# Kernel optimization log

Hardware: AMD Instinct MI355X
Metric: run time of the kernel (lower is better)

## Reference

```python
import jax, jax.numpy as jnp
import numpy as np

D = 768          # embedding_dim
H = 12           # num_heads
DH = 768         # head_dim == embedding_dim (hardcoded in Block)
DF = 4 * D       # FFN hidden
B, S = 4, 1024
EPS = 1e-5


def setup_inputs() -> dict:
    key = jax.random.key(0)
    ks = jax.random.split(key, 20)
    sd = lambda fan_in: 1.0 / np.sqrt(fan_in)
    return {
        "x":  jax.random.normal(ks[0], (B, S, D), jnp.float32),
        # per-head QKV (stacked over head axis)
        "Wq": jax.random.normal(ks[1], (H, D, DH), jnp.float32) * sd(D),
        "bq": jnp.zeros((H, DH), jnp.float32),
        "Wk": jax.random.normal(ks[2], (H, D, DH), jnp.float32) * sd(D),
        "bk": jnp.zeros((H, DH), jnp.float32),
        "Wv": jax.random.normal(ks[3], (H, D, DH), jnp.float32) * sd(D),
        "bv": jnp.zeros((H, DH), jnp.float32),
        # output projection: concat(H*DH) -> D
        "Wo": jax.random.normal(ks[4], (H * DH, D), jnp.float32) * sd(H * DH),
        "bo": jnp.zeros((D,), jnp.float32),
        # feed-forward
        "W1": jax.random.normal(ks[5], (D, DF), jnp.float32) * sd(D),
        "b1": jnp.zeros((DF,), jnp.float32),
        "W2": jax.random.normal(ks[6], (DF, D), jnp.float32) * sd(DF),
        "b2": jnp.zeros((D,), jnp.float32),
        # layer norms
        "g1": jnp.ones((D,), jnp.float32),  "be1": jnp.zeros((D,), jnp.float32),
        "g2": jnp.ones((D,), jnp.float32),  "be2": jnp.zeros((D,), jnp.float32),
    }


def _layernorm(x, g, b):
    mu = jnp.mean(x, axis=-1, keepdims=True)
    var = jnp.mean(jnp.square(x - mu), axis=-1, keepdims=True)
    return (x - mu) * jax.lax.rsqrt(var + EPS) * g + b


def reference(x, Wq, bq, Wk, bk, Wv, bv, Wo, bo, W1, b1, W2, b2, g1, be1, g2, be2):
    h = _layernorm(x, g1, be1)                                   # [B,S,D]
    # per-head projections, stacked over head axis -> [B,H,S,DH]
    Q = jnp.einsum('bsd,hde->bhse', h, Wq) + bq[None, :, None, :]
    K = jnp.einsum('bsd,hde->bhse', h, Wk) + bk[None, :, None, :]
    V = jnp.einsum('bsd,hde->bhse', h, Wv) + bv[None, :, None, :]
    scale = DH ** -0.5
    scores = jnp.einsum('bhse,bhte->bhst', Q, K) * scale          # [B,H,S,S] (no causal mask in source)
    attn = jax.nn.softmax(scores, axis=-1)
    ctx = jnp.einsum('bhst,bhte->bhse', attn, V)                  # [B,H,S,DH]
    concat = ctx.transpose(0, 2, 1, 3).reshape(B, S, H * DH)      # concat heads on last dim
    attn_out = concat @ Wo + bo                                   # dropout: eval identity
    x1 = x + attn_out
    h2 = _layernorm(x1, g2, be2)
    ffn = jax.nn.relu(h2 @ W1 + b1) @ W2 + b2                     # dropout: eval identity
    return x1 + ffn
```

## Files before the change

kernel.cpp:

```cpp
#include <hip/hip_runtime.h>
#include <hip/hip_bf16.h>


typedef __attribute__((ext_vector_type(8))) __bf16 bf16x8;
typedef __attribute__((ext_vector_type(4))) float f32x4;
typedef __attribute__((ext_vector_type(4))) float float4_t;
typedef __attribute__((ext_vector_type(4))) unsigned short ushort4_t;

#define DEV __device__ __forceinline__

DEV unsigned short f2bf(float f) {
    __hip_bfloat16 h = __float2bfloat16(f);
    return *reinterpret_cast<unsigned short*>(&h);
}
DEV float bf2f(unsigned short u) {
    return __uint_as_float(((unsigned int)u) << 16);
}

DEV void gld16(const void* g, void* l) {
    __builtin_amdgcn_global_load_lds(
        (const __attribute__((address_space(1))) void*)g,
        (__attribute__((address_space(3))) void*)l, 16, 0, 0);
}

__global__ __launch_bounds__(256) void f2b_conv(
    const float* __restrict__ in, unsigned short* __restrict__ outb, int n4)
{
    int i = blockIdx.x * 256 + threadIdx.x;
    if (i >= n4) return;
    float4_t v = *(const float4_t*)(in + (size_t)i * 4);
    ushort4_t o;
#pragma unroll
    for (int j = 0; j < 4; j++) o[j] = f2bf(v[j]);
    *(ushort4_t*)(outb + (size_t)i * 4) = o;
}

__global__ __launch_bounds__(256) void transpose_f2b(
    const float* __restrict__ in, unsigned short* __restrict__ outb, int R, int C)
{
    __shared__ float tile[32][33];
    const int c0 = blockIdx.x * 32, r0 = blockIdx.y * 32;
    const int tx = threadIdx.x & 31, ty = threadIdx.x >> 5;
#pragma unroll
    for (int i = 0; i < 32; i += 8)
        tile[ty + i][tx] = in[(size_t)(r0 + ty + i) * C + c0 + tx];
    __syncthreads();
#pragma unroll
    for (int i = 0; i < 32; i += 8)
        outb[(size_t)(c0 + ty + i) * R + r0 + tx] = f2bf(tile[tx][ty + i]);
}

__global__ __launch_bounds__(256) void wk_bq(
    const float* __restrict__ Wk, const float* __restrict__ bq, float* __restrict__ U)
{
    int i = blockIdx.x * 256 + threadIdx.x;
    int h = i / 768;
    const float* wr = Wk + (size_t)i * 768;
    const float* bh = bq + (size_t)h * 768;
    float s = 0.f;
#pragma unroll 4
    for (int e = 0; e < 768; e++) s += wr[e] * bh[e];
    U[i] = s;
}

__global__ __launch_bounds__(256) void bvwo_part(
    const float* __restrict__ Wo, const float* __restrict__ bv, float* __restrict__ part)
{
    int e = blockIdx.x * 256 + threadIdx.x;
    int r0 = blockIdx.y * 96;
    float s = 0.f;
#pragma unroll 4
    for (int r = r0; r < r0 + 96; r++) s += bv[r] * Wo[(size_t)r * 768 + e];
    part[(size_t)blockIdx.y * 768 + e] = s;
}

__global__ __launch_bounds__(256) void bvwo_final(
    const float* __restrict__ part, const float* __restrict__ bo, float* __restrict__ R)
{
    int e = blockIdx.x * 256 + threadIdx.x;
    float s = bo[e];
#pragma unroll
    for (int c = 0; c < 96; c++) s += part[(size_t)c * 768 + e];
    R[e] = s;
}

__global__ __launch_bounds__(256) void layernorm768(
    const float* __restrict__ in, const float* __restrict__ g,
    const float* __restrict__ be, unsigned short* __restrict__ outb)
{
    const size_t rowoff = (size_t)blockIdx.x * 768;
    const float* xr = in + rowoff;
    const int t = threadIdx.x;
    float v0 = xr[t], v1 = xr[t + 256], v2 = xr[t + 512];
    __shared__ float red[8];
    float s = v0 + v1 + v2;
#pragma unroll
    for (int o = 32; o; o >>= 1) s += __shfl_down(s, o);
    if ((t & 63) == 0) red[t >> 6] = s;
    __syncthreads();
    float mu = (red[0] + red[1] + red[2] + red[3]) * (1.0f / 768.0f);
    float d0 = v0 - mu, d1 = v1 - mu, d2 = v2 - mu;
    float q = d0 * d0 + d1 * d1 + d2 * d2;
#pragma unroll
    for (int o = 32; o; o >>= 1) q += __shfl_down(q, o);
    if ((t & 63) == 0) red[4 + (t >> 6)] = q;
    __syncthreads();
    float rs = rsqrtf((red[4] + red[5] + red[6] + red[7]) * (1.0f / 768.0f) + 1e-5f);
    outb[rowoff + t]       = f2bf(d0 * rs * g[t]       + be[t]);
    outb[rowoff + t + 256] = f2bf(d1 * rs * g[t + 256] + be[t + 256]);
    outb[rowoff + t + 512] = f2bf(d2 * rs * g[t + 512] + be[t + 512]);
}

__global__ __launch_bounds__(256) void softmax1024(unsigned short* __restrict__ p)
{
    unsigned short* row = p + (size_t)blockIdx.x * 1024;
    const int t = threadIdx.x;
    ushort4_t uv = *(const ushort4_t*)(row + t * 4);
    float v[4];
    float m = -3.4e38f;
#pragma unroll
    for (int i = 0; i < 4; i++) { v[i] = bf2f(uv[i]); m = fmaxf(m, v[i]); }
    __shared__ float red[8];
#pragma unroll
    for (int o = 32; o; o >>= 1) m = fmaxf(m, __shfl_down(m, o));
    if ((t & 63) == 0) red[t >> 6] = m;
    __syncthreads();
    m = fmaxf(fmaxf(red[0], red[1]), fmaxf(red[2], red[3]));
    float s = 0.f;
#pragma unroll
    for (int i = 0; i < 4; i++) { v[i] = __expf(v[i] - m); s += v[i]; }
#pragma unroll
    for (int o = 32; o; o >>= 1) s += __shfl_down(s, o);
    if ((t & 63) == 0) red[4 + (t >> 6)] = s;
    __syncthreads();
    float inv = 1.f / (red[4] + red[5] + red[6] + red[7]);
    ushort4_t ov;
#pragma unroll
    for (int i = 0; i < 4; i++) ov[i] = f2bf(v[i] * inv);
    *(ushort4_t*)(row + t * 4) = ov;
}

__global__ __launch_bounds__(256) void reduce4(
    const float* __restrict__ res, const float* __restrict__ colb,
    const float* __restrict__ p0, const float* __restrict__ p1,
    const float* __restrict__ p2, const float* __restrict__ p3,
    float* __restrict__ dst)
{
    int i = blockIdx.x * 256 + threadIdx.x;
    float4_t r = *(const float4_t*)(res + (size_t)i * 4);
    float4_t a = *(const float4_t*)(p0 + (size_t)i * 4);
    float4_t b = *(const float4_t*)(p1 + (size_t)i * 4);
    float4_t c = *(const float4_t*)(p2 + (size_t)i * 4);
    float4_t d = *(const float4_t*)(p3 + (size_t)i * 4);
    float4_t cb = *(const float4_t*)(colb + (size_t)(i % 192) * 4);
    float4_t o;
#pragma unroll
    for (int j = 0; j < 4; j++) o[j] = r[j] + cb[j] + (a[j] + b[j]) + (c[j] + d[j]);
    *(float4_t*)(dst + (size_t)i * 4) = o;
}

enum { MODE_BF16 = 0, MODE_VT = 1, MODE_F32RES = 2 };

template <int MODE, bool RELU>
__global__ __launch_bounds__(256) void gemm_bt(
    const unsigned short* __restrict__ A, int lda,
    const unsigned short* __restrict__ Bt, int ldb,
    void* __restrict__ Cout, int ldc,
    const float* __restrict__ bias,
    const float* __restrict__ res, int ldr,
    float scale, int K, int zdiv,
    long long sA1, long long sA2, long long sB1, long long sB2,
    long long sC1, long long sC2, long long sCJ, long long sBias)
{
    const unsigned gx = gridDim.x, gy = gridDim.y;
    const unsigned nwg = gx * gy * gridDim.z;
    unsigned lin = blockIdx.x + gx * (blockIdx.y + gy * blockIdx.z);
    {
        const unsigned q = nwg >> 3, r = nwg & 7;
        const unsigned xcd = lin & 7, idx = lin >> 3;
        lin = (xcd < r ? xcd * (q + 1) : r * (q + 1) + (xcd - r) * q) + idx;
    }
    const unsigned bx = lin % gx;
    const unsigned rem = lin / gx;
    const unsigned by = rem % gy, bz = rem / gy;

    const int z = (int)bz, zq = z / zdiv, zr = z % zdiv;
    A  += (size_t)zq * sA1 + (size_t)zr * sA2;
    Bt += (size_t)zq * sB1 + (size_t)zr * sB2;
    const size_t cOff = (size_t)zq * sC1 + (size_t)(zq >> 1) * sCJ + (size_t)zr * sC2;
    const float* biasp = bias ? bias + (size_t)zr * sBias : nullptr;

    const int m0 = by * 128, n0 = bx * 128;

    __shared__ __align__(16) unsigned short As[2][128 * 32];
    __shared__ __align__(16) unsigned short Bs[2][128 * 32];

    const int t = threadIdx.x, lane = t & 63, wave = t >> 6;
    const int wr = wave >> 1, wc = wave & 1;

    f32x4 zero = {0.f, 0.f, 0.f, 0.f};
    f32x4 acc[4][4];
#pragma unroll
    for (int i = 0; i < 4; i++)
#pragma unroll
        for (int j = 0; j < 4; j++) acc[i][j] = zero;

    const int r0 = t >> 2;
    const int ce = (t & 3) * 8;
    const int kq = (lane >> 4) * 8, rr = lane & 15;

    const int nt = K >> 5;

    auto stage = [&](int buf, int kt) {
        const int kk = kt * 32;
        const unsigned short* ga0 = A  + (size_t)(m0 + r0) * lda      + kk + ce;
        const unsigned short* ga1 = A  + (size_t)(m0 + 64 + r0) * lda + kk + ce;
        const unsigned short* gb0 = Bt + (size_t)(n0 + r0) * ldb      + kk + ce;
        const unsigned short* gb1 = Bt + (size_t)(n0 + 64 + r0) * ldb + kk + ce;
        char* la = (char*)(&As[buf][0]);
        char* lb = (char*)(&Bs[buf][0]);
        gld16(ga0, la + wave * 1024);
        gld16(ga1, la + 4096 + wave * 1024);
        gld16(gb0, lb + wave * 1024);
        gld16(gb1, lb + 4096 + wave * 1024);
    };

    stage(0, 0);
    stage(1, 1);
    asm volatile("s_waitcnt vmcnt(4)" ::: "memory");
    __builtin_amdgcn_s_barrier();

    int cur = 0;
    for (int kt = 0; kt < nt; ++kt) {
        bf16x8 a[4], b[4];
        const unsigned short* Ab = &As[cur][0];
        const unsigned short* Bb = &Bs[cur][0];
#pragma unroll
        for (int i = 0; i < 4; i++) {
            a[i] = *(const bf16x8*)(Ab + (wr * 64 + i * 16 + rr) * 32 + kq);
            b[i] = *(const bf16x8*)(Bb + (wc * 64 + i * 16 + rr) * 32 + kq);
        }
        asm volatile("s_waitcnt lgkmcnt(0)" ::: "memory");
        __builtin_amdgcn_s_barrier();
        if (kt + 2 < nt) stage(cur, kt + 2);

        __builtin_amdgcn_s_setprio(1);
#pragma unroll
        for (int i = 0; i < 4; i++)
#pragma unroll
            for (int j = 0; j < 4; j++)
                acc[i][j] = __builtin_amdgcn_mfma_f32_16x16x32_bf16(a[i], b[j], acc[i][j], 0, 0, 0);
        __builtin_amdgcn_s_setprio(0);

        if (kt + 2 < nt) asm volatile("s_waitcnt vmcnt(4)" ::: "memory");
        else             asm volatile("s_waitcnt vmcnt(0)" ::: "memory");
        __builtin_amdgcn_s_barrier();
        cur ^= 1;
    }

    const int cr = (lane >> 4) * 4, cc = lane & 15;
#pragma unroll
    for (int i = 0; i < 4; i++) {
        const int rowb = m0 + wr * 64 + i * 16 + cr;
#pragma unroll
        for (int j = 0; j < 4; j++) {
            const int col = n0 + wc * 64 + j * 16 + cc;
            const float bv = biasp ? biasp[col] : 0.f;
            if (MODE == MODE_VT) {
                ushort4_t pk;
#pragma unroll
                for (int r = 0; r < 4; r++) {
                    float v = acc[i][j][r] * scale + bv;
                    if (RELU) v = fmaxf(v, 0.f);
                    pk[r] = f2bf(v);
                }
                *(ushort4_t*)((unsigned short*)Cout + cOff +
                              (size_t)col * ldc + rowb) = pk;
            } else {
#pragma unroll
                for (int r = 0; r < 4; r++) {
                    float v = acc[i][j][r] * scale + bv;
                    if (RELU) v = fmaxf(v, 0.f);
                    const int row = rowb + r;
                    if (MODE == MODE_BF16) {
                        ((unsigned short*)Cout)[cOff + (size_t)row * ldc + col] = f2bf(v);
                    } else {
                        float ov = res ? v + res[(size_t)row * ldr + col] : v;
                        ((float*)Cout)[cOff + (size_t)row * ldc + col] = ov;
                    }
                }
            }
        }
    }
}

__global__ void ws_too_small(float* o, float v) { o[0] = v; }

extern "C" void kernel_launch(void* const* d_in, const int* in_sizes, int n_in,
                              void* d_out, int out_size, void* d_ws, size_t ws_size,
                              hipStream_t stream)
{
    const float* x   = (const float*)d_in[0];
    const float* Wq  = (const float*)d_in[1];
    const float* bq  = (const float*)d_in[2];
    const float* Wk  = (const float*)d_in[3];
    const float* Wv  = (const float*)d_in[5];
    const float* bv  = (const float*)d_in[6];
    const float* Wo  = (const float*)d_in[7];
    const float* bo  = (const float*)d_in[8];
    const float* W1  = (const float*)d_in[9];
    const float* b1  = (const float*)d_in[10];
    const float* W2  = (const float*)d_in[11];
    const float* b2  = (const float*)d_in[12];
    const float* g1  = (const float*)d_in[13];
    const float* be1 = (const float*)d_in[14];
    const float* g2  = (const float*)d_in[15];
    const float* be2 = (const float*)d_in[16];
    float* out = (float*)d_out;

    char* ws = (char*)d_ws;
    unsigned short* W1T  = (unsigned short*)(ws);
    unsigned short* W2T  = (unsigned short*)(ws + 4718592);
    unsigned short* WQKT = (unsigned short*)(ws + 9437184);
    unsigned short* WVOT = (unsigned short*)(ws + 23592960);
    float*          U    = (float*)(ws + 37748736);
    float*          BVWO = (float*)(ws + 37785600);
    float*          PART = (float*)(ws + 37788672);
    unsigned short* HB   = (unsigned short*)(ws + 38083584);
    float*          X1   = (float*)(ws + 44375040);
    unsigned short* TB   = (unsigned short*)(ws + 56957952);
    unsigned short* SC   = (unsigned short*)(ws + 132455424);
    const size_t NEED = 258284544;

    if (ws_size < NEED) {
        hipMemsetAsync(d_out, 0, (size_t)out_size * sizeof(float), stream);
        ws_too_small<<<1, 1, 0, stream>>>(out, (float)ws_size);
        return;
    }

    unsigned short* VOT = TB;
    float* P0 = (float*)(ws + 9437184);
    float* P1 = (float*)(ws + 22020096);
    float* P2 = (float*)(ws + 233118720);
    float* P3 = (float*)(ws + 245701632);
    unsigned short* WqB = (unsigned short*)(ws + 132455424);
    unsigned short* WkB = (unsigned short*)(ws + 146611200);
    unsigned short* WvB = (unsigned short*)(ws + 160766976);
    unsigned short* WOT = (unsigned short*)(ws + 174922752);
    unsigned short* H2B = (unsigned short*)(ws + 56957952);
    unsigned short* FFN = (unsigned short*)(ws + 63249408);

    f2b_conv<<<6912, 256, 0, stream>>>(Wq, WqB, 1769472);
    f2b_conv<<<6912, 256, 0, stream>>>(Wk, WkB, 1769472);
    f2b_conv<<<6912, 256, 0, stream>>>(Wv, WvB, 1769472);
    transpose_f2b<<<dim3(24, 288), 256, 0, stream>>>(Wo, WOT, 9216, 768);
    transpose_f2b<<<dim3(96, 24), 256, 0, stream>>>(W1, W1T, 768, 3072);
    transpose_f2b<<<dim3(24, 96), 256, 0, stream>>>(W2, W2T, 3072, 768);

    gemm_bt<MODE_BF16, false><<<dim3(6, 6, 12), 256, 0, stream>>>(
        WkB, 768, WqB, 768, WQKT, 768, nullptr, nullptr, 0, 1.0f, 768, 12,
        0, 589824, 0, 589824, 0, 589824, 0, 0);
    gemm_bt<MODE_BF16, false><<<dim3(6, 6, 12), 256, 0, stream>>>(
        WOT, 9216, WvB, 768, WVOT, 768, nullptr, nullptr, 0, 1.0f, 768, 12,
        0, 768, 0, 589824, 0, 589824, 0, 0);

    wk_bq<<<36, 256, 0, stream>>>(Wk, bq, U);
    bvwo_part<<<dim3(3, 96), 256, 0, stream>>>(Wo, bv, PART);
    bvwo_final<<<3, 256, 0, stream>>>(PART, bo, BVWO);

    layernorm768<<<4096, 256, 0, stream>>>(x, g1, be1, HB);

    gemm_bt<MODE_BF16, false><<<dim3(6, 8, 48), 256, 0, stream>>>(
        HB, 768, WQKT, 768, TB, 768, U, nullptr, 0, 1.0f, 768, 12,
        786432, 0, 0, 589824, 9437184, 786432, 0, 768);

    gemm_bt<MODE_BF16, false><<<dim3(8, 8, 48), 256, 0, stream>>>(
        TB, 768, HB, 768, SC, 12288, nullptr, nullptr, 0,
        0.03608439182435161f, 768, 12,
        9437184, 786432, 786432, 0, 12582912, 1024, 0, 0);

    softmax1024<<<49152, 256, 0, stream>>>(SC);

    gemm_bt<MODE_VT, false><<<dim3(6, 8, 48), 256, 0, stream>>>(
        HB, 768, WVOT, 768, VOT, 12288, nullptr, nullptr, 0, 1.0f, 768, 12,
        786432, 0, 0, 589824, 9437184, 1024, 0, 0);

    gemm_bt<MODE_F32RES, false><<<dim3(6, 8, 16), 256, 0, stream>>>(
        SC, 12288, VOT, 12288, P0, 768, nullptr, nullptr, 0, 1.0f, 3072, 4,
        3072, 12582912, 3072, 9437184, 3145728, 786432, 49628928, 0);

    reduce4<<<3072, 256, 0, stream>>>(x, BVWO, P0, P1, P2, P3, X1);

    layernorm768<<<4096, 256, 0, stream>>>(X1, g2, be2, H2B);

    gemm_bt<MODE_BF16, true><<<dim3(24, 32, 1), 256, 0, stream>>>(
        H2B, 768, W1T, 768, FFN, 3072, b1, nullptr, 0, 1.0f, 768, 1,
        0, 0, 0, 0, 0, 0, 0, 0);

    gemm_bt<MODE_F32RES, false><<<dim3(6, 32, 4), 256, 0, stream>>>(
        FFN, 3072, W2T, 3072, P0, 768, nullptr, nullptr, 0, 1.0f, 768, 1,
        768, 0, 768, 0, 3145728, 0, 49628928, 0);

    reduce4<<<3072, 256, 0, stream>>>(X1, b2, P0, P1, P2, P3, out);
}
```

Measured before the change: 673.6 us.

## Add 256x256-tile 8-wave GEMM kernel with 4-stage pipeline for activation GEMMs

Adds a new bf16 MFMA GEMM kernel that uses 256x256 output tiles, 512 threads (8 waves), and a four-buffer global-to-LDS pipeline. Loads for A and B are interleaved with two MFMA half-steps, and setprio raises wave priority during the MFMA sections. All per-forward activation GEMMs switch to this kernel with correspondingly smaller grids. The larger tiles are meant to increase operand reuse and cut global traffic per FLOP, at the cost of fewer workgroups, more LDS and register pressure, and possible wave-quantization imbalance on the smaller grids.

```diff
diff --git a/kernel.cpp b/kernel.cpp
--- a/kernel.cpp
+++ b/kernel.cpp
@@ -160,6 +160,152 @@
 }
 
 enum { MODE_BF16 = 0, MODE_VT = 1, MODE_F32RES = 2 };
+
+template <int MODE, bool RELU>
+__global__ __launch_bounds__(512, 2) void gemm256(
+    const unsigned short* __restrict__ A, int lda,
+    const unsigned short* __restrict__ Bt, int ldb,
+    void* __restrict__ Cout, int ldc,
+    const float* __restrict__ bias,
+    const float* __restrict__ res, int ldr,
+    float scale, int K, int zdiv,
+    long long sA1, long long sA2, long long sB1, long long sB2,
+    long long sC1, long long sC2, long long sCJ, long long sBias)
+{
+    const unsigned gx = gridDim.x, gy = gridDim.y;
+    const unsigned nwg = gx * gy * gridDim.z;
+    unsigned lin = blockIdx.x + gx * (blockIdx.y + gy * blockIdx.z);
+    {
+        const unsigned q = nwg >> 3, r = nwg & 7;
+        const unsigned xcd = lin & 7, idx = lin >> 3;
+        lin = (xcd < r ? xcd * (q + 1) : r * (q + 1) + (xcd - r) * q) + idx;
+    }
+    const unsigned bx = lin % gx;
+    const unsigned rem = lin / gx;
+    const unsigned by = rem % gy, bz = rem / gy;
+
+    const int z = (int)bz, zq = z / zdiv, zr = z % zdiv;
+    A  += (size_t)zq * sA1 + (size_t)zr * sA2;
+    Bt += (size_t)zq * sB1 + (size_t)zr * sB2;
+    const size_t cOff = (size_t)zq * sC1 + (size_t)(zq >> 1) * sCJ + (size_t)zr * sC2;
+    const float* biasp = bias ? bias + (size_t)zr * sBias : nullptr;
+
+    const int m0 = by * 256, n0 = bx * 256;
+
+    __shared__ __align__(16) unsigned short As[4][8192];
+    __shared__ __align__(16) unsigned short Bs[4][8192];
+
+    const int t = threadIdx.x, lane = t & 63, wave = t >> 6;
+    const int wm = wave >> 2, wn = wave & 3;
+    const int rr = lane & 15, g8 = (lane >> 4) * 8;
+    const int sr = t >> 2, sc = (t & 3) * 8;
+
+    f32x4 zero = {0.f, 0.f, 0.f, 0.f};
+    f32x4 acc[8][4];
+#pragma unroll
+    for (int i = 0; i < 8; i++)
+#pragma unroll
+        for (int j = 0; j < 4; j++) acc[i][j] = zero;
+
+    const int NT = K >> 5;
+
+    auto stageA = [&](int kt) {
+        const int kk = (kt << 5) + sc;
+        char* l = ((char*)&As[kt & 3][0]) + (wave << 10);
+        gld16(A + (size_t)(m0 + sr) * lda + kk,       l);
+        gld16(A + (size_t)(m0 + 128 + sr) * lda + kk, l + 8192);
+    };
+    auto stageB = [&](int kt) {
+        const int kk = (kt << 5) + sc;
+        char* l = ((char*)&Bs[kt & 3][0]) + (wave << 10);
+        gld16(Bt + (size_t)(n0 + sr) * ldb + kk,       l);
+        gld16(Bt + (size_t)(n0 + 128 + sr) * ldb + kk, l + 8192);
+    };
+
+    stageA(0); stageB(0);
+    stageA(1); stageB(1);
+    stageA(2); stageB(2);
+    asm volatile("s_waitcnt vmcnt(8)" ::: "memory");
+    __builtin_amdgcn_s_barrier();
+
+    for (int kt = 0; kt < NT; ++kt) {
+        const unsigned short* Abuf = &As[kt & 3][0];
+        const unsigned short* Bbuf = &Bs[kt & 3][0];
+        bf16x8 afr[4], bfr[4];
+
+#pragma unroll
+        for (int j = 0; j < 4; j++)
+            bfr[j] = *(const bf16x8*)(Bbuf + (wn * 64 + j * 16 + rr) * 32 + g8);
+#pragma unroll
+        for (int f = 0; f < 4; f++)
+            afr[f] = *(const bf16x8*)(Abuf + (wm * 128 + f * 16 + rr) * 32 + g8);
+        if (kt + 3 < NT) stageA(kt + 3);
+        __builtin_amdgcn_s_barrier();
+        __builtin_amdgcn_s_setprio(1);
+#pragma unroll
+        for (int f = 0; f < 4; f++)
+#pragma unroll
+            for (int j = 0; j < 4; j++)
+                acc[f][j] = __builtin_amdgcn_mfma_f32_16x16x32_bf16(afr[f], bfr[j], acc[f][j], 0, 0, 0);
+        __builtin_amdgcn_s_setprio(0);
+        __builtin_amdgcn_s_barrier();
+
+#pragma unroll
+        for (int f = 0; f < 4; f++)
+            afr[f] = *(const bf16x8*)(Abuf + (wm * 128 + 64 + f * 16 + rr) * 32 + g8);
+        if (kt + 3 < NT) stageB(kt + 3);
+        __builtin_amdgcn_s_barrier();
+        __builtin_amdgcn_s_setprio(1);
+#pragma unroll
+        for (int f = 0; f < 4; f++)
+#pragma unroll
+            for (int j = 0; j < 4; j++)
+                acc[4 + f][j] = __builtin_amdgcn_mfma_f32_16x16x32_bf16(afr[f], bfr[j], acc[4 + f][j], 0, 0, 0);
+        __builtin_amdgcn_s_setprio(0);
+
+        if (kt < NT - 1) {
+            if (kt < NT - 3)       asm volatile("s_waitcnt vmcnt(8)" ::: "memory");
+            else if (kt == NT - 3) asm volatile("s_waitcnt vmcnt(4)" ::: "memory");
+            else                   asm volatile("s_waitcnt vmcnt(0)" ::: "memory");
+            __builtin_amdgcn_s_barrier();
+        }
+    }
+
+    const int cr = (lane >> 4) * 4, cc = lane & 15;
+#pragma unroll
+    for (int i = 0; i < 8; i++) {
+        const int rowb = m0 + wm * 128 + i * 16 + cr;
+#pragma unroll
+        for (int j = 0; j < 4; j++) {
+            const int col = n0 + wn * 64 + j * 16 + cc;
+            const float bv = biasp ? biasp[col] : 0.f;
+            if (MODE == MODE_VT) {
+                ushort4_t pk;
+#pragma unroll
+                for (int r = 0; r < 4; r++) {
+                    float v = acc[i][j][r] * scale + bv;
+                    if (RELU) v = fmaxf(v, 0.f);
+                    pk[r] = f2bf(v);
+                }
+                *(ushort4_t*)((unsigned short*)Cout + cOff +
+                              (size_t)col * ldc + rowb) = pk;
+            } else {
+#pragma unroll
+                for (int r = 0; r < 4; r++) {
+                    float v = acc[i][j][r] * scale + bv;
+                    if (RELU) v = fmaxf(v, 0.f);
+                    const int row = rowb + r;
+                    if (MODE == MODE_BF16) {
+                        ((unsigned short*)Cout)[cOff + (size_t)row * ldc + col] = f2bf(v);
+                    } else {
+                        float ov = res ? v + res[(size_t)row * ldr + col] : v;
+                        ((float*)Cout)[cOff + (size_t)row * ldc + col] = ov;
+                    }
+                }
+            }
+        }
+    }
+}
 
 template <int MODE, bool RELU>
 __global__ __launch_bounds__(256) void gemm_bt(
@@ -370,22 +516,22 @@
 
     layernorm768<<<4096, 256, 0, stream>>>(x, g1, be1, HB);
 
-    gemm_bt<MODE_BF16, false><<<dim3(6, 8, 48), 256, 0, stream>>>(
+    gemm256<MODE_BF16, false><<<dim3(3, 4, 48), 512, 0, stream>>>(
         HB, 768, WQKT, 768, TB, 768, U, nullptr, 0, 1.0f, 768, 12,
         786432, 0, 0, 589824, 9437184, 786432, 0, 768);
 
-    gemm_bt<MODE_BF16, false><<<dim3(8, 8, 48), 256, 0, stream>>>(
+    gemm256<MODE_BF16, false><<<dim3(4, 4, 48), 512, 0, stream>>>(
         TB, 768, HB, 768, SC, 12288, nullptr, nullptr, 0,
         0.03608439182435161f, 768, 12,
         9437184, 786432, 786432, 0, 12582912, 1024, 0, 0);
 
     softmax1024<<<49152, 256, 0, stream>>>(SC);
 
-    gemm_bt<MODE_VT, false><<<dim3(6, 8, 48), 256, 0, stream>>>(
+    gemm256<MODE_VT, false><<<dim3(3, 4, 48), 512, 0, stream>>>(
         HB, 768, WVOT, 768, VOT, 12288, nullptr, nullptr, 0, 1.0f, 768, 12,
         786432, 0, 0, 589824, 9437184, 1024, 0, 0);
 
-    gemm_bt<MODE_F32RES, false><<<dim3(6, 8, 16), 256, 0, stream>>>(
+    gemm256<MODE_F32RES, false><<<dim3(3, 4, 16), 512, 0, stream>>>(
         SC, 12288, VOT, 12288, P0, 768, nullptr, nullptr, 0, 1.0f, 3072, 4,
         3072, 12582912, 3072, 9437184, 3145728, 786432, 49628928, 0);
 
@@ -393,11 +539,11 @@
 
     layernorm768<<<4096, 256, 0, stream>>>(X1, g2, be2, H2B);
 
-    gemm_bt<MODE_BF16, true><<<dim3(24, 32, 1), 256, 0, stream>>>(
+    gemm256<MODE_BF16, true><<<dim3(12, 16, 1), 512, 0, stream>>>(
         H2B, 768, W1T, 768, FFN, 3072, b1, nullptr, 0, 1.0f, 768, 1,
         0, 0, 0, 0, 0, 0, 0, 0);
 
-    gemm_bt<MODE_F32RES, false><<<dim3(6, 32, 4), 256, 0, stream>>>(
+    gemm256<MODE_F32RES, false><<<dim3(3, 16, 4), 512, 0, stream>>>(
         FFN, 3072, W2T, 3072, P0, 768, nullptr, nullptr, 0, 1.0f, 768, 1,
         768, 0, 768, 0, 3145728, 0, 49628928, 0);
 
```

Measured after the change: 707.1 us. 5.0% more time.
